# Kernel optimization log

Hardware: AMD Instinct MI355X
Metric: run time of the kernel (lower is better)

## Reference

```python
import jax, jax.numpy as jnp
import numpy as np


def setup_inputs() -> dict:
    key = jax.random.key(0)
    ks = jax.random.split(key, 5)
    B, S, D, U = 4, 2048, 1024, 1024
    scale = 1.0 / np.sqrt(D)
    return {
        "query": jax.random.normal(ks[0], (B, S, D), dtype=jnp.float32),
        "value": jax.random.normal(ks[1], (B, S, D), dtype=jnp.float32),
        "Wq": jax.random.normal(ks[2], (D, U), dtype=jnp.float32) * scale,
        "bq": jnp.zeros((U,), dtype=jnp.float32),
        "Wk": jax.random.normal(ks[3], (D, U), dtype=jnp.float32) * scale,
        "bk": jnp.zeros((U,), dtype=jnp.float32),
        "Wv": jax.random.normal(ks[4], (D, U), dtype=jnp.float32) * scale,
        "bv": jnp.zeros((U,), dtype=jnp.float32),
    }


def reference(query, value, Wq, bq, Wk, bk, Wv, bv):
    # Dense projections (last-dim matmul + bias)
    Q = jnp.einsum("bsd,du->bsu", query, Wq) + bq   # [B,Sq,U]
    K = jnp.einsum("btd,du->btu", value, Wk) + bk   # [B,Sk,U]
    V = jnp.einsum("btd,du->btu", value, Wv) + bv   # [B,Sk,U]
    d_k = jnp.asarray(K.shape[-1], dtype=jnp.float32)
    scores = jnp.einsum("bsu,btu->bst", Q, K) / jnp.sqrt(d_k)  # [B,Sq,Sk]
    weights = jax.nn.softmax(scores, axis=-1)
    return jnp.einsum("bst,btu->bsu", weights, V)   # [B,Sq,U]
```

## Files before the change

kernel.cpp:

```cpp
#include <hip/hip_runtime.h>
#include <hip/hip_bf16.h>
#include <stdint.h>

#define DEVINL __device__ __forceinline__

typedef __attribute__((ext_vector_type(4))) float f32x4;
typedef __attribute__((ext_vector_type(8))) __bf16 bfv8;
typedef __attribute__((ext_vector_type(8))) short s16x8;
typedef __attribute__((ext_vector_type(4))) short s16x4;

DEVINL short f2bf(float f) {
  union { float f; unsigned u; } v; v.f = f;
  unsigned r = v.u + 0x7FFFu + ((v.u >> 16) & 1u);
  return (short)(r >> 16);
}
DEVINL float bf2f(short h) {
  union { unsigned u; float f; } v; v.u = ((unsigned)(unsigned short)h) << 16;
  return v.f;
}
DEVINL void gload_lds16(const void* g, void* l) {
  __builtin_amdgcn_global_load_lds((__attribute__((address_space(1))) unsigned*)(g),
                                   (__attribute__((address_space(3))) unsigned*)(l),
                                   16, 0, 0);
}
#define S_BARRIER() __builtin_amdgcn_s_barrier()
#define MEMORD() asm volatile("" ::: "memory")
template <int N> DEVINL void vmwaitc() {
  asm volatile("s_waitcnt vmcnt(%0)" :: "i"(N) : "memory");
}
DEVINL int xswz(int p, int n) { return (p & 7) * (n >> 3) + (p >> 3); }

template <int BU, int NF, int RING>
DEVINL void gemm_core(const short* __restrict__ Ag, const short* __restrict__ Bg,
                      int lda, int ldb, int m0, int n0, int nkt,
                      short* lds, f32x4 (&acc)[8][NF]) {
  constexpr int U = 2 + BU;
  constexpr int SLOT = 8192 + BU * 4096;
  const int tid = threadIdx.x;
  const int w = tid >> 6, l = tid & 63;
  const int wm = w >> 2, wn = w & 3;
  const int lr = l & 15, lg = l >> 4;
  const int stg_row = w * 16 + (l >> 2);
  const int stg_col = (((l & 3) ^ ((l >> 3) & 3)) << 3);
  const int ck = ((lg ^ ((lr >> 1) & 3)) << 3);
  const int aro = (wm * 128 + lr) * 32 + ck;
  const int bro = 8192 + (wn * (NF * 16) + lr) * 32 + ck;
  const int dW = w * 512;
#define STAGE_A(t) { short* S_ = lds + ((t) % RING) * SLOT;                                \
    gload_lds16(Ag + (size_t)(m0 + stg_row) * lda + (t) * 32 + stg_col, S_ + dW);          \
    gload_lds16(Ag + (size_t)(m0 + 128 + stg_row) * lda + (t) * 32 + stg_col,              \
                S_ + 4096 + dW); }
#define STAGE_B(t) { short* S_ = lds + ((t) % RING) * SLOT;                                \
    _Pragma("unroll")                                                                      \
    for (int u_ = 0; u_ < BU; ++u_)                                                        \
      gload_lds16(Bg + (size_t)(n0 + u_ * 128 + stg_row) * ldb + (t) * 32 + stg_col,       \
                  S_ + 8192 + u_ * 4096 + dW); }
#pragma unroll
  for (int t = 0; t < RING - 1; ++t) { STAGE_A(t); STAGE_B(t); }
  vmwaitc<(RING - 2) * U>(); S_BARRIER(); MEMORD();
  bfv8 aA[4], aB[4], bA[NF], bB[NF];
  {
    const short* Sp = lds;
#pragma unroll
    for (int mf = 0; mf < 4; ++mf) aA[mf] = *(const bfv8*)(Sp + aro + mf * 512);
#pragma unroll
    for (int nf = 0; nf < NF; ++nf) bA[nf] = *(const bfv8*)(Sp + bro + nf * 512);
  }
#pragma unroll 1
  for (int kt = 0; kt < nkt; kt += 2) {
    const short* S1 = lds + ((kt + 1) % RING) * SLOT;
    const short* S2 = lds + ((kt + 2) % RING) * SLOT;
    const short* S0 = lds + (kt % RING) * SLOT;
    if (kt + 2 < nkt) STAGE_A(kt + 2);
#pragma unroll
    for (int mf = 0; mf < 4; ++mf) aB[mf] = *(const bfv8*)(S0 + aro + 2048 + mf * 512);
#pragma unroll
    for (int mf = 0; mf < 4; ++mf)
#pragma unroll
      for (int nf = 0; nf < NF; ++nf)
        acc[mf][nf] = __builtin_amdgcn_mfma_f32_16x16x32_bf16(aA[mf], bA[nf], acc[mf][nf], 0, 0, 0);
    if (kt + 2 < nkt) vmwaitc<2>(); else vmwaitc<0>();
    S_BARRIER(); MEMORD();
    if (kt + 2 < nkt) STAGE_B(kt + 2);
#pragma unroll
    for (int mf = 0; mf < 4; ++mf) aA[mf] = *(const bfv8*)(S1 + aro + mf * 512);
#pragma unroll
    for (int nf = 0; nf < NF; ++nf) bB[nf] = *(const bfv8*)(S1 + bro + nf * 512);
#pragma unroll
    for (int mf = 0; mf < 4; ++mf)
#pragma unroll
      for (int nf = 0; nf < NF; ++nf)
        acc[4 + mf][nf] = __builtin_amdgcn_mfma_f32_16x16x32_bf16(aB[mf], bA[nf], acc[4 + mf][nf], 0, 0, 0);
    S_BARRIER(); MEMORD();
    if (kt + 3 < nkt) STAGE_A(kt + 3);
#pragma unroll
    for (int mf = 0; mf < 4; ++mf) aB[mf] = *(const bfv8*)(S1 + aro + 2048 + mf * 512);
#pragma unroll
    for (int mf = 0; mf < 4; ++mf)
#pragma unroll
      for (int nf = 0; nf < NF; ++nf)
        acc[mf][nf] = __builtin_amdgcn_mfma_f32_16x16x32_bf16(aA[mf], bB[nf], acc[mf][nf], 0, 0, 0);
    if (kt + 3 < nkt) vmwaitc<2>(); else vmwaitc<0>();
    S_BARRIER(); MEMORD();
    if (kt + 3 < nkt) STAGE_B(kt + 3);
    if (kt + 2 < nkt) {
#pragma unroll
      for (int mf = 0; mf < 4; ++mf) aA[mf] = *(const bfv8*)(S2 + aro + mf * 512);
#pragma unroll
      for (int nf = 0; nf < NF; ++nf) bA[nf] = *(const bfv8*)(S2 + bro + nf * 512);
    }
#pragma unroll
    for (int mf = 0; mf < 4; ++mf)
#pragma unroll
      for (int nf = 0; nf < NF; ++nf)
        acc[4 + mf][nf] = __builtin_amdgcn_mfma_f32_16x16x32_bf16(aB[mf], bB[nf], acc[4 + mf][nf], 0, 0, 0);
    S_BARRIER(); MEMORD();
  }
#undef STAGE_A
#undef STAGE_B
}

__global__ __launch_bounds__(256) void prep_kernel(
    const float* __restrict__ q, const float* __restrict__ v,
    const float* __restrict__ Wq, const float* __restrict__ Wk, const float* __restrict__ Wv,
    short* __restrict__ Qc, short* __restrict__ Vc,
    short* __restrict__ Wqc, short* __restrict__ Wkc, short* __restrict__ WTv) {
  __shared__ float tile[64][65];
  const int bx = blockIdx.x;
  if (bx < 9216) {
    const float* src; short* dst; int off;
    if (bx < 4096)      { src = q;  dst = Qc;  off = bx; }
    else if (bx < 8192) { src = v;  dst = Vc;  off = bx - 4096; }
    else if (bx < 8704) { src = Wq; dst = Wqc; off = bx - 8192; }
    else                { src = Wk; dst = Wkc; off = bx - 8704; }
    const size_t i = ((size_t)off * 256 + threadIdx.x) * 8;
    f32x4 x0 = *(const f32x4*)(src + i);
    f32x4 x1 = *(const f32x4*)(src + i + 4);
    s16x8 o;
#pragma unroll
    for (int j = 0; j < 4; ++j) { o[j] = f2bf(x0[j]); o[4 + j] = f2bf(x1[j]); }
    *(s16x8*)(dst + i) = o;
  } else {
    const int xx = bx - 9216;
    const int k0 = (xx & 15) << 6, n0 = (xx >> 4) << 6;
    const int c = threadIdx.x & 63, r0 = threadIdx.x >> 6;
#pragma unroll
    for (int i = 0; i < 16; ++i) {
      int r = (i << 2) + r0;
      tile[r][c] = Wv[(size_t)(k0 + r) * 1024 + n0 + c];
    }
    __syncthreads();
#pragma unroll
    for (int i = 0; i < 16; ++i) {
      int a = (i << 2) + r0;
      WTv[(size_t)(n0 + a) * 1024 + k0 + c] = f2bf(tile[c][a]);
    }
  }
}

__global__ __launch_bounds__(256) void bias0_kernel(const float* __restrict__ Wk,
                                                    const float* __restrict__ bq,
                                                    float* __restrict__ v1,
                                                    float* __restrict__ flagp) {
  __shared__ float red[256];
  const int t = threadIdx.x;
  float any = 0.f;
  for (int i = t; i < 1024; i += 256) any += fabsf(bq[i]);
  red[t] = any; __syncthreads();
  for (int s = 128; s > 0; s >>= 1) { if (t < s) red[t] += red[t + s]; __syncthreads(); }
  const float fl = red[0];
  if (t == 0) *flagp = fl;
  if (fl != 0.f) {
    for (int r = t; r < 1024; r += 256) {
      float acc = 0.f;
      for (int u = 0; u < 1024; ++u) acc += Wk[(size_t)r * 1024 + u] * bq[u];
      v1[r] = acc;
    }
  }
}

__global__ __launch_bounds__(256) void tvec_kernel(const float* __restrict__ Y,
                                                   const float* __restrict__ v1,
                                                   const float* __restrict__ flagp,
                                                   float* __restrict__ tvec) {
  const int t = blockIdx.x * 256 + threadIdx.x;
  if (*flagp == 0.f) { tvec[t] = 0.f; return; }
  float acc = 0.f;
  for (int d = 0; d < 1024; ++d) acc += Y[(size_t)t * 1024 + d] * v1[d];
  tvec[t] = acc;
}

__global__ __launch_bounds__(512, 2) void mker_kernel(const short* __restrict__ Wkc,
                                                      const short* __restrict__ Wqc,
                                                      float* __restrict__ Part) {
  __shared__ short lds[36864];
  const int o = xswz(blockIdx.x, 128);
  const int ks = o >> 5, r = o & 31;
  const int bm = r >> 3, bn = r & 7;
  const int m0 = bm * 256, n0 = bn * 128;
  f32x4 acc[8][2];
#pragma unroll
  for (int i = 0; i < 8; ++i)
#pragma unroll
    for (int j = 0; j < 2; ++j) acc[i][j] = (f32x4){0.f, 0.f, 0.f, 0.f};
  gemm_core<1, 2, 3>(Wkc + ks * 256, Wqc + ks * 256, 1024, 1024, m0, n0, 8, lds, acc);
  float* O = Part + (size_t)ks * 1048576;
  const int l = threadIdx.x & 63, w = threadIdx.x >> 6;
  const int wm = w >> 2, wn = w & 3, lr = l & 15, lg = l >> 4;
#pragma unroll
  for (int i = 0; i < 8; ++i) {
    const int row0 = m0 + wm * 128 + (i >> 2) * 64 + (i & 3) * 16 + lg * 4;
#pragma unroll
    for (int nf = 0; nf < 2; ++nf) {
      const int col = n0 + wn * 32 + nf * 16 + lr;
#pragma unroll
      for (int j = 0; j < 4; ++j)
        O[(size_t)(row0 + j) * 1024 + col] = acc[i][nf][j];
    }
  }
}

__global__ __launch_bounds__(256) void mkred_kernel(const float* __restrict__ Part,
                                                    short* __restrict__ MT) {
  const size_t i = ((size_t)blockIdx.x * 256 + threadIdx.x) * 4;
  f32x4 a = *(const f32x4*)(Part + i);
  f32x4 b = *(const f32x4*)(Part + 1048576 + i);
  f32x4 c = *(const f32x4*)(Part + 2097152 + i);
  f32x4 d = *(const f32x4*)(Part + 3145728 + i);
  s16x4 o;
#pragma unroll
  for (int j = 0; j < 4; ++j) o[j] = f2bf(a[j] + b[j] + c[j] + d[j]);
  *(s16x4*)(MT + i) = o;
}

__global__ __launch_bounds__(512, 2) void qproj_kernel(const short* __restrict__ Qc,
                                                       const short* __restrict__ MT,
                                                       short* __restrict__ Ap) {
  __shared__ short lds[36864];
  const int o = xswz(blockIdx.x, 256);
  const int bm = o >> 3, bn = o & 7;
  const int m0 = bm * 256, n0 = bn * 128;
  f32x4 acc[8][2];
#pragma unroll
  for (int i = 0; i < 8; ++i)
#pragma unroll
    for (int j = 0; j < 2; ++j) acc[i][j] = (f32x4){0.f, 0.f, 0.f, 0.f};
  gemm_core<1, 2, 3>(Qc, MT, 1024, 1024, m0, n0, 32, lds, acc);
  const int l = threadIdx.x & 63, w = threadIdx.x >> 6;
  const int wm = w >> 2, wn = w & 3, lr = l & 15, lg = l >> 4;
#pragma unroll
  for (int i = 0; i < 8; ++i) {
    const int row0 = m0 + wm * 128 + (i >> 2) * 64 + (i & 3) * 16 + lg * 4;
#pragma unroll
    for (int nf = 0; nf < 2; ++nf) {
      const int col = n0 + wn * 32 + nf * 16 + lr;
#pragma unroll
      for (int j = 0; j < 4; ++j)
        Ap[(size_t)(row0 + j) * 1024 + col] = f2bf(acc[i][nf][j]);
    }
  }
}

__global__ __launch_bounds__(512, 2) void vproj_kernel(
    const short* __restrict__ Vc, const short* __restrict__ WTv,
    const float* __restrict__ bv, short* __restrict__ VT) {
  __shared__ short lds[36864];
  const int o = xswz(blockIdx.x, 256);
  const int bm = o >> 3, bn = o & 7;
  const int m0 = bm * 256, n0 = bn * 128;
  f32x4 acc[8][2];
#pragma unroll
  for (int i = 0; i < 8; ++i)
#pragma unroll
    for (int j = 0; j < 2; ++j) acc[i][j] = (f32x4){0.f, 0.f, 0.f, 0.f};
  gemm_core<1, 2, 3>(Vc, WTv, 1024, 1024, m0, n0, 32, lds, acc);
  const int tid = threadIdx.x;
  const int w = tid >> 6, l = tid & 63;
  const int wm = w >> 2, wn = w & 3, lr = l & 15, lg = l >> 4;
  __syncthreads();
  short* lt = lds;
#pragma unroll
  for (int i = 0; i < 8; ++i) {
    const int tl = wm * 128 + (i >> 2) * 64 + (i & 3) * 16 + lg * 4;
#pragma unroll
    for (int nf = 0; nf < 2; ++nf) {
      const int ul = wn * 32 + nf * 16 + lr;
      const float bb = bv[n0 + ul];
      s16x4 pk;
#pragma unroll
      for (int j = 0; j < 4; ++j) pk[j] = f2bf(acc[i][nf][j] + bb);
      *(s16x4*)&lt[ul * 264 + tl] = pk;
    }
  }
  __syncthreads();
  const int b = m0 >> 11, t0 = m0 & 2047;
#pragma unroll
  for (int it = 0; it < 8; ++it) {
    const int cid = it * 512 + tid;
    const int u = cid >> 5, tc = cid & 31;
    s16x8 v8 = *(const s16x8*)&lt[u * 264 + tc * 8];
    *(s16x8*)(VT + ((size_t)b * 1024 + n0 + u) * 2048 + t0 + tc * 8) = v8;
  }
}

__global__ __launch_bounds__(512, 4) void qkt_kernel(const short* __restrict__ Ap,
                                                     const short* __restrict__ Vc,
                                                     const float* __restrict__ tvec,
                                                     short* __restrict__ sb0,
                                                     short* __restrict__ sb3) {
  __shared__ short lds[36864];
  const int o = xswz(blockIdx.x, 512);
  const int bt = o >> 7, r = o & 127;
  const int bm = r >> 4, bn = r & 15;
  const short* A = Ap + (size_t)bt * 2097152;
  const short* B = Vc + (size_t)bt * 2097152;
  short* O = (bt < 3) ? (sb0 + (size_t)bt * 4194304) : sb3;
  const int m0 = bm * 256, n0 = bn * 128;
  f32x4 acc[8][2];
#pragma unroll
  for (int i = 0; i < 8; ++i)
#pragma unroll
    for (int j = 0; j < 2; ++j) acc[i][j] = (f32x4){0.f, 0.f, 0.f, 0.f};
  gemm_core<1, 2, 3>(A, B, 1024, 1024, m0, n0, 32, lds, acc);
  const int tid = threadIdx.x;
  const int w = tid >> 6, l = tid & 63;
  const int wm = w >> 2, wn = w & 3, lr = l & 15, lg = l >> 4;
  float tv[2];
#pragma unroll
  for (int nf = 0; nf < 2; ++nf) tv[nf] = tvec[bt * 2048 + n0 + wn * 32 + nf * 16 + lr];
#pragma unroll
  for (int i = 0; i < 8; ++i) {
    const int row0 = m0 + wm * 128 + (i >> 2) * 64 + (i & 3) * 16 + lg * 4;
#pragma unroll
    for (int nf = 0; nf < 2; ++nf) {
      const int col = n0 + wn * 32 + nf * 16 + lr;
#pragma unroll
      for (int j = 0; j < 4; ++j)
        O[(size_t)(row0 + j) * 2048 + col] = f2bf((acc[i][nf][j] + tv[nf]) * 0.03125f);
    }
  }
}

__global__ __launch_bounds__(512, 2) void pv_kernel(const short* __restrict__ sb0,
                                                    const short* __restrict__ sb3,
                                                    const short* __restrict__ VT,
                                                    float* __restrict__ Out) {
  __shared__ short lds[36864];
  const int o = xswz(blockIdx.x, 256);
  const int bt = o >> 6, r = o & 63;
  const int bm = r >> 3, bn = r & 7;
  const short* A = (bt < 3) ? (sb0 + (size_t)bt * 4194304) : sb3;
  const short* B = VT + (size_t)bt * 2097152;
  float* O = Out + (size_t)bt * 2097152;
  const int m0 = bm * 256, n0 = bn * 128;
  f32x4 acc[8][2];
#pragma unroll
  for (int i = 0; i < 8; ++i)
#pragma unroll
    for (int j = 0; j < 2; ++j) acc[i][j] = (f32x4){0.f, 0.f, 0.f, 0.f};
  gemm_core<1, 2, 3>(A, B, 2048, 2048, m0, n0, 64, lds, acc);
  const int l = threadIdx.x & 63, w = threadIdx.x >> 6;
  const int wm = w >> 2, wn = w & 3, lr = l & 15, lg = l >> 4;
#pragma unroll
  for (int i = 0; i < 8; ++i) {
    const int row0 = m0 + wm * 128 + (i >> 2) * 64 + (i & 3) * 16 + lg * 4;
#pragma unroll
    for (int nf = 0; nf < 2; ++nf) {
      const int col = n0 + wn * 32 + nf * 16 + lr;
#pragma unroll
      for (int j = 0; j < 4; ++j)
        O[(size_t)(row0 + j) * 1024 + col] = acc[i][nf][j];
    }
  }
}

__global__ __launch_bounds__(256) void softmax_kernel(short* __restrict__ sb0,
                                                      short* __restrict__ sb3) {
  const int row = blockIdx.x;
  const int bt = row >> 11;
  short* p = ((bt < 3) ? (sb0 + (size_t)bt * 4194304) : sb3) + (size_t)(row & 2047) * 2048;
  const int tid = threadIdx.x;
  const int w = tid >> 6, l = tid & 63;
  s16x8 v = *(const s16x8*)(p + tid * 8);
  float f[8];
#pragma unroll
  for (int j = 0; j < 8; ++j) f[j] = bf2f(v[j]);
  float m = f[0];
#pragma unroll
  for (int j = 1; j < 8; ++j) m = fmaxf(m, f[j]);
#pragma unroll
  for (int o = 32; o > 0; o >>= 1) m = fmaxf(m, __shfl_xor(m, o, 64));
  __shared__ float redm[4], reds[4];
  if (l == 0) redm[w] = m;
  __syncthreads();
  m = fmaxf(fmaxf(redm[0], redm[1]), fmaxf(redm[2], redm[3]));
  float s = 0.f;
#pragma unroll
  for (int j = 0; j < 8; ++j) { f[j] = __expf(f[j] - m); s += f[j]; }
#pragma unroll
  for (int o = 32; o > 0; o >>= 1) s += __shfl_xor(s, o, 64);
  if (l == 0) reds[w] = s;
  __syncthreads();
  s = reds[0] + reds[1] + reds[2] + reds[3];
  const float inv = 1.f / s;
  s16x8 o8;
#pragma unroll
  for (int j = 0; j < 8; ++j) o8[j] = f2bf(f[j] * inv);
  *(s16x8*)(p + tid * 8) = o8;
}

extern "C" void kernel_launch(void* const* d_in, const int* in_sizes, int n_in,
                              void* d_out, int out_size, void* d_ws, size_t ws_size,
                              hipStream_t stream) {
  const float* query = (const float*)d_in[0];
  const float* value = (const float*)d_in[1];
  const float* Wq = (const float*)d_in[2];
  const float* bq = (const float*)d_in[3];
  const float* Wk = (const float*)d_in[4];
  const float* Wv = (const float*)d_in[6];
  const float* bv = (const float*)d_in[7];

  char* ws = (char*)d_ws;
  short* Wqc = (short*)(ws);
  short* Wkc = (short*)(ws + ((size_t)2 << 20));
  short* MT  = (short*)(ws + ((size_t)4 << 20));
  short* WTv = (short*)(ws + ((size_t)6 << 20));
  short* Qc  = (short*)(ws + ((size_t)8 << 20));
  short* Vc  = (short*)(ws + ((size_t)24 << 20));
  float* Part = (float*)(ws + ((size_t)40 << 20));
  short* Ap  = (short*)(ws + ((size_t)40 << 20));
  short* VT  = (short*)(ws + ((size_t)56 << 20));
  short* sb0 = (short*)(ws);
  short* sb3 = (short*)(ws + ((size_t)72 << 20));
  float* tvec = (float*)(ws + ((size_t)80 << 20));
  float* v1   = (float*)(ws + ((size_t)80 << 20) + 65536);
  float* flagp = (float*)(ws + ((size_t)80 << 20) + 131072);

  prep_kernel<<<dim3(9472), 256, 0, stream>>>(query, value, Wq, Wk, Wv,
                                              Qc, Vc, Wqc, Wkc, WTv);
  bias0_kernel<<<dim3(1), 256, 0, stream>>>(Wk, bq, v1, flagp);
  tvec_kernel<<<dim3(32), 256, 0, stream>>>(value, v1, flagp, tvec);

  mker_kernel<<<dim3(128), 512, 0, stream>>>(Wkc, Wqc, Part);
  mkred_kernel<<<dim3(1024), 256, 0, stream>>>(Part, MT);

  qproj_kernel<<<dim3(256), 512, 0, stream>>>(Qc, MT, Ap);
  vproj_kernel<<<dim3(256), 512, 0, stream>>>(Vc, WTv, bv, VT);

  qkt_kernel<<<dim3(512), 512, 0, stream>>>(Ap, Vc, tvec, sb0, sb3);
  softmax_kernel<<<dim3(8192), 256, 0, stream>>>(sb0, sb3);
  pv_kernel<<<dim3(256), 512, 0, stream>>>(sb0, sb3, VT, (float*)d_out);
}
```

Baseline: 189.4 us.

## Merge Q and V projection launches and split PV GEMM along K

Merges the Q-projection and V-projection GEMMs into one 512-block launch that branches on block index, so both fill the GPU at once. Splits the PV GEMM into two K halves across 512 blocks. One half writes directly to the output and the other writes a fp32 partial buffer, which a new add kernel then sums. The aim is to raise occupancy and parallelism on small 256-block grids, in exchange for an extra 32 MB partial write/read pass and one more launch. Launch bounds are also raised to 4 blocks per CU.

```diff
diff --git a/kernel.cpp b/kernel.cpp
--- a/kernel.cpp
+++ b/kernel.cpp
@@ -233,73 +233,62 @@
   *(s16x4*)(MT + i) = o;
 }
 
-__global__ __launch_bounds__(512, 2) void qproj_kernel(const short* __restrict__ Qc,
-                                                       const short* __restrict__ MT,
-                                                       short* __restrict__ Ap) {
-  __shared__ short lds[36864];
-  const int o = xswz(blockIdx.x, 256);
-  const int bm = o >> 3, bn = o & 7;
-  const int m0 = bm * 256, n0 = bn * 128;
-  f32x4 acc[8][2];
-#pragma unroll
-  for (int i = 0; i < 8; ++i)
-#pragma unroll
-    for (int j = 0; j < 2; ++j) acc[i][j] = (f32x4){0.f, 0.f, 0.f, 0.f};
-  gemm_core<1, 2, 3>(Qc, MT, 1024, 1024, m0, n0, 32, lds, acc);
-  const int l = threadIdx.x & 63, w = threadIdx.x >> 6;
-  const int wm = w >> 2, wn = w & 3, lr = l & 15, lg = l >> 4;
-#pragma unroll
-  for (int i = 0; i < 8; ++i) {
-    const int row0 = m0 + wm * 128 + (i >> 2) * 64 + (i & 3) * 16 + lg * 4;
-#pragma unroll
-    for (int nf = 0; nf < 2; ++nf) {
-      const int col = n0 + wn * 32 + nf * 16 + lr;
-#pragma unroll
-      for (int j = 0; j < 4; ++j)
-        Ap[(size_t)(row0 + j) * 1024 + col] = f2bf(acc[i][nf][j]);
-    }
-  }
-}
-
-__global__ __launch_bounds__(512, 2) void vproj_kernel(
+__global__ __launch_bounds__(512, 4) void qvproj_kernel(
+    const short* __restrict__ Qc, const short* __restrict__ MT, short* __restrict__ Ap,
     const short* __restrict__ Vc, const short* __restrict__ WTv,
     const float* __restrict__ bv, short* __restrict__ VT) {
   __shared__ short lds[36864];
-  const int o = xswz(blockIdx.x, 256);
-  const int bm = o >> 3, bn = o & 7;
+  const int o = xswz(blockIdx.x, 512);
+  const int sel = o >> 8, r = o & 255;
+  const int bm = r >> 3, bn = r & 7;
   const int m0 = bm * 256, n0 = bn * 128;
   f32x4 acc[8][2];
 #pragma unroll
   for (int i = 0; i < 8; ++i)
 #pragma unroll
     for (int j = 0; j < 2; ++j) acc[i][j] = (f32x4){0.f, 0.f, 0.f, 0.f};
-  gemm_core<1, 2, 3>(Vc, WTv, 1024, 1024, m0, n0, 32, lds, acc);
   const int tid = threadIdx.x;
   const int w = tid >> 6, l = tid & 63;
   const int wm = w >> 2, wn = w & 3, lr = l & 15, lg = l >> 4;
-  __syncthreads();
-  short* lt = lds;
-#pragma unroll
-  for (int i = 0; i < 8; ++i) {
-    const int tl = wm * 128 + (i >> 2) * 64 + (i & 3) * 16 + lg * 4;
-#pragma unroll
-    for (int nf = 0; nf < 2; ++nf) {
-      const int ul = wn * 32 + nf * 16 + lr;
-      const float bb = bv[n0 + ul];
-      s16x4 pk;
-#pragma unroll
-      for (int j = 0; j < 4; ++j) pk[j] = f2bf(acc[i][nf][j] + bb);
-      *(s16x4*)&lt[ul * 264 + tl] = pk;
-    }
-  }
-  __syncthreads();
-  const int b = m0 >> 11, t0 = m0 & 2047;
-#pragma unroll
-  for (int it = 0; it < 8; ++it) {
-    const int cid = it * 512 + tid;
-    const int u = cid >> 5, tc = cid & 31;
-    s16x8 v8 = *(const s16x8*)&lt[u * 264 + tc * 8];
-    *(s16x8*)(VT + ((size_t)b * 1024 + n0 + u) * 2048 + t0 + tc * 8) = v8;
+  if (sel == 0) {
+    gemm_core<1, 2, 3>(Qc, MT, 1024, 1024, m0, n0, 32, lds, acc);
+#pragma unroll
+    for (int i = 0; i < 8; ++i) {
+      const int row0 = m0 + wm * 128 + (i >> 2) * 64 + (i & 3) * 16 + lg * 4;
+#pragma unroll
+      for (int nf = 0; nf < 2; ++nf) {
+        const int col = n0 + wn * 32 + nf * 16 + lr;
+#pragma unroll
+        for (int j = 0; j < 4; ++j)
+          Ap[(size_t)(row0 + j) * 1024 + col] = f2bf(acc[i][nf][j]);
+      }
+    }
+  } else {
+    gemm_core<1, 2, 3>(Vc, WTv, 1024, 1024, m0, n0, 32, lds, acc);
+    __syncthreads();
+    short* lt = lds;
+#pragma unroll
+    for (int i = 0; i < 8; ++i) {
+      const int tl = wm * 128 + (i >> 2) * 64 + (i & 3) * 16 + lg * 4;
+#pragma unroll
+      for (int nf = 0; nf < 2; ++nf) {
+        const int ul = wn * 32 + nf * 16 + lr;
+        const float bb = bv[n0 + ul];
+        s16x4 pk;
+#pragma unroll
+        for (int j = 0; j < 4; ++j) pk[j] = f2bf(acc[i][nf][j] + bb);
+        *(s16x4*)&lt[ul * 264 + tl] = pk;
+      }
+    }
+    __syncthreads();
+    const int b = m0 >> 11, t0 = m0 & 2047;
+#pragma unroll
+    for (int it = 0; it < 8; ++it) {
+      const int cid = it * 512 + tid;
+      const int u = cid >> 5, tc = cid & 31;
+      s16x8 v8 = *(const s16x8*)&lt[u * 264 + tc * 8];
+      *(s16x8*)(VT + ((size_t)b * 1024 + n0 + u) * 2048 + t0 + tc * 8) = v8;
+    }
   }
 }
 
@@ -341,24 +330,26 @@
   }
 }
 
-__global__ __launch_bounds__(512, 2) void pv_kernel(const short* __restrict__ sb0,
+__global__ __launch_bounds__(512, 4) void pv_kernel(const short* __restrict__ sb0,
                                                     const short* __restrict__ sb3,
                                                     const short* __restrict__ VT,
-                                                    float* __restrict__ Out) {
+                                                    float* __restrict__ Out,
+                                                    float* __restrict__ Part) {
   __shared__ short lds[36864];
-  const int o = xswz(blockIdx.x, 256);
-  const int bt = o >> 6, r = o & 63;
-  const int bm = r >> 3, bn = r & 7;
-  const short* A = (bt < 3) ? (sb0 + (size_t)bt * 4194304) : sb3;
-  const short* B = VT + (size_t)bt * 2097152;
-  float* O = Out + (size_t)bt * 2097152;
+  const int o = xswz(blockIdx.x, 512);
+  const int kh = o >> 8;
+  const int bt = (o >> 6) & 3;
+  const int bm = (o >> 3) & 7, bn = o & 7;
+  const short* A = ((bt < 3) ? (sb0 + (size_t)bt * 4194304) : sb3) + kh * 1024;
+  const short* B = VT + (size_t)bt * 2097152 + kh * 1024;
+  float* O = (kh ? Part : Out) + (size_t)bt * 2097152;
   const int m0 = bm * 256, n0 = bn * 128;
   f32x4 acc[8][2];
 #pragma unroll
   for (int i = 0; i < 8; ++i)
 #pragma unroll
     for (int j = 0; j < 2; ++j) acc[i][j] = (f32x4){0.f, 0.f, 0.f, 0.f};
-  gemm_core<1, 2, 3>(A, B, 2048, 2048, m0, n0, 64, lds, acc);
+  gemm_core<1, 2, 3>(A, B, 2048, 2048, m0, n0, 32, lds, acc);
   const int l = threadIdx.x & 63, w = threadIdx.x >> 6;
   const int wm = w >> 2, wn = w & 3, lr = l & 15, lg = l >> 4;
 #pragma unroll
@@ -372,6 +363,16 @@
         O[(size_t)(row0 + j) * 1024 + col] = acc[i][nf][j];
     }
   }
+}
+
+__global__ __launch_bounds__(256) void add_kernel(float* __restrict__ Out,
+                                                  const float* __restrict__ Part) {
+  const size_t i = ((size_t)blockIdx.x * 256 + threadIdx.x) * 4;
+  f32x4 a = *(const f32x4*)(Out + i);
+  f32x4 b = *(const f32x4*)(Part + i);
+#pragma unroll
+  for (int j = 0; j < 4; ++j) a[j] += b[j];
+  *(f32x4*)(Out + i) = a;
 }
 
 __global__ __launch_bounds__(256) void softmax_kernel(short* __restrict__ sb0,
@@ -427,11 +428,12 @@
   short* WTv = (short*)(ws + ((size_t)6 << 20));
   short* Qc  = (short*)(ws + ((size_t)8 << 20));
   short* Vc  = (short*)(ws + ((size_t)24 << 20));
-  float* Part = (float*)(ws + ((size_t)40 << 20));
+  float* MPart = (float*)(ws + ((size_t)40 << 20));
   short* Ap  = (short*)(ws + ((size_t)40 << 20));
   short* VT  = (short*)(ws + ((size_t)56 << 20));
   short* sb0 = (short*)(ws);
   short* sb3 = (short*)(ws + ((size_t)72 << 20));
+  float* PvPart = (float*)(ws + ((size_t)24 << 20));
   float* tvec = (float*)(ws + ((size_t)80 << 20));
   float* v1   = (float*)(ws + ((size_t)80 << 20) + 65536);
   float* flagp = (float*)(ws + ((size_t)80 << 20) + 131072);
@@ -441,13 +443,14 @@
   bias0_kernel<<<dim3(1), 256, 0, stream>>>(Wk, bq, v1, flagp);
   tvec_kernel<<<dim3(32), 256, 0, stream>>>(value, v1, flagp, tvec);
 
-  mker_kernel<<<dim3(128), 512, 0, stream>>>(Wkc, Wqc, Part);
-  mkred_kernel<<<dim3(1024), 256, 0, stream>>>(Part, MT);
-
-  qproj_kernel<<<dim3(256), 512, 0, stream>>>(Qc, MT, Ap);
-  vproj_kernel<<<dim3(256), 512, 0, stream>>>(Vc, WTv, bv, VT);
+  mker_kernel<<<dim3(128), 512, 0, stream>>>(Wkc, Wqc, MPart);
+  mkred_kernel<<<dim3(1024), 256, 0, stream>>>(MPart, MT);
+
+  qvproj_kernel<<<dim3(512), 512, 0, stream>>>(Qc, MT, Ap, Vc, WTv, bv, VT);
 
   qkt_kernel<<<dim3(512), 512, 0, stream>>>(Ap, Vc, tvec, sb0, sb3);
   softmax_kernel<<<dim3(8192), 256, 0, stream>>>(sb0, sb3);
-  pv_kernel<<<dim3(256), 512, 0, stream>>>(sb0, sb3, VT, (float*)d_out);
-}
+
+  pv_kernel<<<dim3(512), 512, 0, stream>>>(sb0, sb3, VT, (float*)d_out, PvPart);
+  add_kernel<<<dim3(8192), 256, 0, stream>>>((float*)d_out, PvPart);
+}
```

After: 211.8 us. +11.8%, slower.
